# Performance work log

Hardware: AMD Instinct MI355X
Metric: run time of the kernel (lower is better)

## Reference

```python
import jax, jax.numpy as jnp
import numpy as np

B, T, C = 2, 2048, 2048
H, D = 16, 128  # num_heads, head_dim


def setup_inputs() -> dict:
    key = jax.random.key(0)
    ks = jax.random.split(key, 5)
    x = jax.random.normal(ks[0], (B, T, C), dtype=jnp.float32)
    # causal mask: mask==0 positions are filled with -inf
    mask = jnp.tril(jnp.ones((T, T), dtype=jnp.int32))[None, None, :, :]
    wq = jax.random.normal(ks[1], (C, C), dtype=jnp.float32) * (C ** -0.5)
    wk = jax.random.normal(ks[2], (C, C), dtype=jnp.float32) * (C ** -0.5)
    wv = jax.random.normal(ks[3], (C, C), dtype=jnp.float32) * (C ** -0.5)
    wo = jax.random.normal(ks[4], (C, C), dtype=jnp.float32) * (C ** -0.5)
    return {"x": x, "mask": mask, "wq": wq, "wk": wk, "wv": wv, "wo": wo}


def reference(x, mask, wq, wk, wv, wo):
    Bx, Tx, Cx = x.shape
    scale = D ** -0.5
    # torch Linear: y = x @ W.T (weights are [out, in])
    q = (x @ wq.T).reshape(Bx, Tx, H, D).transpose(0, 2, 1, 3)  # [B,H,T,D]
    k = (x @ wk.T).reshape(Bx, Tx, H, D).transpose(0, 2, 1, 3)
    v = (x @ wv.T).reshape(Bx, Tx, H, D).transpose(0, 2, 1, 3)
    scores = jnp.einsum("bhqd,bhkd->bhqk", q, k) * scale  # [B,H,T,T]
    scores = jnp.where(mask == 0, -jnp.inf, scores)
    attn = jax.nn.softmax(scores, axis=-1)
    out = jnp.einsum("bhqk,bhkd->bhqd", attn, v)  # [B,H,T,D]
    out = out.transpose(0, 2, 1, 3).reshape(Bx, Tx, Cx)
    return out @ wo.T
```

## Files before the change

kernel.cpp:

```cpp
#include <hip/hip_runtime.h>
#include <hip/hip_bf16.h>


#define BB 2
#define TT 2048
#define CC 2048
#define HH 16
#define DD 128
#define MM (BB*TT)
#define NQT (TT/64)
#define GNT (CC/64)

typedef __bf16 bf16x8 __attribute__((ext_vector_type(8)));
typedef __bf16 bf16x4 __attribute__((ext_vector_type(4)));
typedef float  f32x4  __attribute__((ext_vector_type(4)));

#define MFMA16(a, b, c) __builtin_amdgcn_mfma_f32_16x16x32_bf16((a), (b), (c), 0, 0, 0)

__device__ __forceinline__ void g2lds16(const void* g, void* l) {
    __builtin_amdgcn_global_load_lds(
        (const __attribute__((address_space(1))) void*)g,
        (__attribute__((address_space(3))) void*)l,
        16, 0, 0);
}

__global__ __launch_bounds__(256) void cvt_all(
    const float* __restrict__ x,  const float* __restrict__ wq,
    const float* __restrict__ wk, const float* __restrict__ wv,
    const float* __restrict__ wo, __bf16* __restrict__ out_base)
{
    const int idx = blockIdx.x * 256 + threadIdx.x;
    const float* in; int off;
    if (idx < (1 << 21)) { in = x; off = idx; }
    else {
        const int r = idx - (1 << 21);
        const int k = r >> 20;
        in  = (k == 0) ? wq : (k == 1) ? wk : (k == 2) ? wv : wo;
        off = r & ((1 << 20) - 1);
    }
    const float4 v = ((const float4*)in)[off];
    bf16x4 o;
    o.x = (__bf16)v.x; o.y = (__bf16)v.y;
    o.z = (__bf16)v.z; o.w = (__bf16)v.w;
    ((bf16x4*)out_base)[idx] = o;
}

template<int MODE>
__global__ __launch_bounds__(512, 2) void gemm_bt(
    const __bf16* __restrict__ A, const __bf16* __restrict__ Wt,
    void* __restrict__ out)
{
    __shared__ __align__(16) __bf16 As[3][256*64];
    __shared__ __align__(16) __bf16 Bs[3][2][128*32];

    const int tid = threadIdx.x;
    const int w   = tid >> 6, lane = tid & 63;
    const int wm  = w >> 1,  wn  = w & 1;
    const int lo  = lane & 15, hi = lane >> 4;
    const int xr  = (lo & 7) << 4;
    const int xb2 = ((lo >> 1) & 3) << 4;

    const int bid   = blockIdx.y * gridDim.x + blockIdx.x;
    const int xcd   = bid & 7, loc = bid >> 3;
    const int n0    = (2*xcd + (loc & 1)) * 128;
    const int m0    = (loc >> 1) * 256;

    const int ar   = tid >> 3, as_ = tid & 7;
    const int acol = ((as_ ^ (ar & 7)) << 3);
    const int br   = tid >> 2, bs_ = tid & 3;
    const int bcol = ((bs_ ^ ((br >> 1) & 3)) << 3);

    auto stageA3a = [&](int buf, int kt) {
        #pragma unroll
        for (int j = 0; j < 3; ++j)
            g2lds16(A + (size_t)(m0 + j*64 + ar)*CC + kt*64 + acol,
                    (char*)&As[buf][0] + j*8192 + w*1024);
    };
    auto stageA3b = [&](int buf, int kt) {
        g2lds16(A + (size_t)(m0 + 3*64 + ar)*CC + kt*64 + acol,
                (char*)&As[buf][0] + 3*8192 + w*1024);
        #pragma unroll
        for (int kh = 0; kh < 2; ++kh)
            g2lds16(Wt + (size_t)(n0 + br)*CC + kt*64 + kh*32 + bcol,
                    (char*)&Bs[buf][kh][0] + w*1024);
    };
    auto rdA = [&](bf16x8* af, int buf, int ks) {
        const char* base = (const char*)&As[buf][0];
        #pragma unroll
        for (int mf = 0; mf < 4; ++mf) {
            const int r = wm*64 + mf*16 + lo;
            af[mf] = *(const bf16x8*)(base + r*128 + ((ks*64 + hi*16) ^ xr));
        }
    };
    auto rdB = [&](bf16x8* bv, int buf, int ks) {
        const char* base = (const char*)&Bs[buf][ks][0];
        #pragma unroll
        for (int nf = 0; nf < 4; ++nf) {
            const int n = wn*64 + nf*16 + lo;
            bv[nf] = *(const bf16x8*)(base + n*64 + ((hi*16) ^ xb2));
        }
    };

    f32x4 acc[4][4] = {};

    stageA3a(0, 0); stageA3b(0, 0);
    stageA3a(1, 1); stageA3b(1, 1);
    asm volatile("s_waitcnt vmcnt(6)" ::: "memory");
    __builtin_amdgcn_s_barrier();

    int rb = 0;
    #pragma unroll 1
    for (int t = 0; t < GNT - 2; ++t) {
        const int sb = (rb == 0) ? 2 : rb - 1;
        {
            bf16x8 af[4], bv[4];
            rdA(af, rb, 0); rdB(bv, rb, 0);
            stageA3a(sb, t + 2);
            __builtin_amdgcn_s_setprio(1);
            #pragma unroll
            for (int mf = 0; mf < 4; ++mf)
                #pragma unroll
                for (int nf = 0; nf < 4; ++nf)
                    acc[mf][nf] = MFMA16(af[mf], bv[nf], acc[mf][nf]);
            __builtin_amdgcn_s_setprio(0);
        }
        {
            bf16x8 af[4], bv[4];
            rdA(af, rb, 1); rdB(bv, rb, 1);
            stageA3b(sb, t + 2);
            __builtin_amdgcn_s_setprio(1);
            #pragma unroll
            for (int mf = 0; mf < 4; ++mf)
                #pragma unroll
                for (int nf = 0; nf < 4; ++nf)
                    acc[mf][nf] = MFMA16(af[mf], bv[nf], acc[mf][nf]);
            __builtin_amdgcn_s_setprio(0);
            asm volatile("s_waitcnt vmcnt(6)" ::: "memory");
            __builtin_amdgcn_s_barrier();
        }
        rb = (rb == 2) ? 0 : rb + 1;
    }
    {
        bf16x8 af[4], bv[4];
        rdA(af, rb, 0); rdB(bv, rb, 0);
        #pragma unroll
        for (int mf = 0; mf < 4; ++mf)
            #pragma unroll
            for (int nf = 0; nf < 4; ++nf)
                acc[mf][nf] = MFMA16(af[mf], bv[nf], acc[mf][nf]);
        rdA(af, rb, 1); rdB(bv, rb, 1);
        #pragma unroll
        for (int mf = 0; mf < 4; ++mf)
            #pragma unroll
            for (int nf = 0; nf < 4; ++nf)
                acc[mf][nf] = MFMA16(af[mf], bv[nf], acc[mf][nf]);
        asm volatile("s_waitcnt vmcnt(0)" ::: "memory");
        __builtin_amdgcn_s_barrier();
        rb = (rb == 2) ? 0 : rb + 1;
    }
    {
        bf16x8 af[4], bv[4];
        rdA(af, rb, 0); rdB(bv, rb, 0);
        #pragma unroll
        for (int mf = 0; mf < 4; ++mf)
            #pragma unroll
            for (int nf = 0; nf < 4; ++nf)
                acc[mf][nf] = MFMA16(af[mf], bv[nf], acc[mf][nf]);
        rdA(af, rb, 1); rdB(bv, rb, 1);
        #pragma unroll
        for (int mf = 0; mf < 4; ++mf)
            #pragma unroll
            for (int nf = 0; nf < 4; ++nf)
                acc[mf][nf] = MFMA16(af[mf], bv[nf], acc[mf][nf]);
    }

    #pragma unroll
    for (int mf = 0; mf < 4; ++mf) {
        #pragma unroll
        for (int nf = 0; nf < 4; ++nf) {
            #pragma unroll
            for (int r = 0; r < 4; ++r) {
                const int row = m0 + wm*64 + mf*16 + hi*4 + r;
                const int col = n0 + wn*64 + nf*16 + lo;
                const float v = acc[mf][nf][r];
                if (MODE == 0) {
                    const int b = row >> 11, t = row & (TT-1);
                    const int h = col >> 7,  d = col & (DD-1);
                    ((__bf16*)out)[(size_t)((b*HH + h)*TT + t)*DD + d] = (__bf16)v;
                } else if (MODE == 1) {
                    const int b = row >> 11, t = row & (TT-1);
                    const int h = col >> 7,  d = col & (DD-1);
                    ((__bf16*)out)[(size_t)((b*HH + h)*DD + d)*TT + t] = (__bf16)v;
                } else {
                    ((float*)out)[(size_t)row*CC + col] = v;
                }
            }
        }
    }
}

__global__ __launch_bounds__(256, 2) void attn_fwd(
    const __bf16* __restrict__ Q, const __bf16* __restrict__ K,
    const __bf16* __restrict__ Vt, __bf16* __restrict__ O)
{
    __shared__ __align__(16) __bf16 Ks[2][64*128];
    __shared__ __align__(16) __bf16 Vs[2][128*64];
    __shared__ __align__(16) __bf16 Ps[4][16*64];

    const int lid   = blockIdx.y * gridDim.x + blockIdx.x;
    const int bh    = lid & 31;
    const int pairx = lid >> 5;
    const int tid = threadIdx.x;
    const int w   = tid >> 6, lane = tid & 63;
    const int lo  = lane & 15, hi = lane >> 4;
    const int xr  = (lo & 7) << 4;

    const int krow_l  = lane >> 4;
    const int kcol_sw = ((lane & 15) << 4);
    const int vrow_l  = lane >> 3;
    const int vcol_sw = (((lane & 7) ^ (lane >> 3)) << 3);

    const size_t kbase = (size_t)bh * TT * DD;
    const size_t vbase = (size_t)bh * DD * TT;
    const int b = bh >> 4, h = bh & 15;
    const float SC = 0.12754613142f;

    bf16x8 vones;
    #pragma unroll
    for (int i = 0; i < 8; ++i) vones[i] = (__bf16)1.0f;

    auto stage = [&](int buf, int kv0) {
        #pragma unroll
        for (int i = 0; i < 4; ++i) {
            const int c = 4*w + i;
            {
                const int row = 4*c + krow_l;
                const int sw  = (kcol_sw ^ ((row & 7) << 4)) >> 1;
                g2lds16(K + kbase + (size_t)(kv0 + row)*DD + sw,
                        &Ks[buf][0] + c*512);
            }
            {
                const int row = 8*c + vrow_l;
                g2lds16(Vt + vbase + (size_t)row*TT + kv0 + vcol_sw,
                        &Vs[buf][0] + c*512);
            }
        }
    };

    #pragma unroll 1
    for (int half = 0; half < 2; ++half) {
        const int qt = half ? pairx : (NQT - 1 - pairx);
        const int q0 = qt * 64;

        const __bf16* Qbase = Q + (kbase + (size_t)(q0 + w*16 + lo) * DD);
        bf16x8 qf[4];
        #pragma unroll
        for (int kc = 0; kc < 4; ++kc)
            qf[kc] = *(const bf16x8*)(Qbase + kc*32 + hi*8);

        float mrow[4];
        #pragma unroll
        for (int r = 0; r < 4; ++r) mrow[r] = -1e30f;
        f32x4 oacc[8] = {};
        f32x4 sacc = {};

        const int qg_base = q0 + w*16 + hi*4;
        const int ntiles  = qt + 1;

        stage(0, 0);
        __syncthreads();
        int cur = 0;

        for (int t = 0; t < ntiles; ++t) {
            const int kv0 = t*64;
            if (t + 1 < ntiles) stage(cur ^ 1, (t+1)*64);

            const char* Kb = (const char*)&Ks[cur][0];
            const char* Vb = (const char*)&Vs[cur][0];

            f32x4 s[4];
            __builtin_amdgcn_s_setprio(1);
            #pragma unroll
            for (int st = 0; st < 4; ++st) {
                f32x4 a = {};
                #pragma unroll
                for (int kc = 0; kc < 4; ++kc) {
                    const bf16x8 kf = *(const bf16x8*)(
                        Kb + (st*16 + lo)*256 + ((kc*64 + hi*16) ^ xr));
                    a = MFMA16(qf[kc], kf, a);
                }
                s[st] = a;
            }
            __builtin_amdgcn_s_setprio(0);

            float pmax[4];
            const bool diag = (t == ntiles - 1);
            #pragma unroll
            for (int r = 0; r < 4; ++r) {
                const int qg = qg_base + r;
                float mx = -1e30f;
                #pragma unroll
                for (int st = 0; st < 4; ++st) {
                    float v = s[st][r] * SC;
                    if (diag) {
                        const int kvg = kv0 + st*16 + lo;
                        v = (kvg > qg) ? -1e30f : v;
                    }
                    s[st][r] = v;
                    mx = fmaxf(mx, v);
                }
                #pragma unroll
                for (int msk = 1; msk < 16; msk <<= 1)
                    mx = fmaxf(mx, __shfl_xor(mx, msk, 64));
                pmax[r] = mx;
            }

            bool need = false;
            #pragma unroll
            for (int r = 0; r < 4; ++r)
                need = need || (pmax[r] > mrow[r] + 11.5f);
            if (__any(need)) {
                float rsc[4];
                #pragma unroll
                for (int r = 0; r < 4; ++r) {
                    const float mnew = fmaxf(mrow[r], pmax[r]);
                    rsc[r]  = __builtin_amdgcn_exp2f(mrow[r] - mnew);
                    mrow[r] = mnew;
                    sacc[r] *= rsc[r];
                }
                #pragma unroll
                for (int dc = 0; dc < 8; ++dc)
                    #pragma unroll
                    for (int r = 0; r < 4; ++r)
                        oacc[dc][r] *= rsc[r];
            }

            #pragma unroll
            for (int r = 0; r < 4; ++r)
                #pragma unroll
                for (int st = 0; st < 4; ++st)
                    s[st][r] = __builtin_amdgcn_exp2f(s[st][r] - mrow[r]);

            char* Pw = (char*)&Ps[w][0];
            #pragma unroll
            for (int st = 0; st < 4; ++st)
                #pragma unroll
                for (int r = 0; r < 4; ++r) {
                    const int row = hi*4 + r;
                    *(__bf16*)(Pw + row*128 + (((st*16 + lo)*2) ^ ((row & 7) << 4)))
                        = (__bf16)s[st][r];
                }

            __builtin_amdgcn_s_setprio(1);
            #pragma unroll
            for (int kc2 = 0; kc2 < 2; ++kc2) {
                const bf16x8 pf = *(const bf16x8*)(
                    Pw + lo*128 + ((kc2*64 + hi*16) ^ xr));
                #pragma unroll
                for (int dc = 0; dc < 8; ++dc) {
                    const bf16x8 vf = *(const bf16x8*)(
                        Vb + (dc*16 + lo)*128 + ((kc2*64 + hi*16) ^ xr));
                    oacc[dc] = MFMA16(pf, vf, oacc[dc]);
                }
                sacc = MFMA16(pf, vones, sacc);
            }
            __builtin_amdgcn_s_setprio(0);

            __syncthreads();
            cur ^= 1;
        }

        #pragma unroll
        for (int r = 0; r < 4; ++r) {
            const float inv = 1.f / sacc[r];
            const int qg = qg_base + r;
            #pragma unroll
            for (int dc = 0; dc < 8; ++dc) {
                const int d = dc*16 + lo;
                O[(size_t)(b*TT + qg)*CC + h*DD + d] = (__bf16)(oacc[dc][r] * inv);
            }
        }
    }
}

extern "C" void kernel_launch(void* const* d_in, const int* in_sizes, int n_in,
                              void* d_out, int out_size, void* d_ws, size_t ws_size,
                              hipStream_t stream) {
    const float* x  = (const float*)d_in[0];
    const float* wq = (const float*)d_in[2];
    const float* wk = (const float*)d_in[3];
    const float* wv = (const float*)d_in[4];
    const float* wo = (const float*)d_in[5];

    char* p = (char*)d_ws;
    __bf16* xb  = (__bf16*)p; p += (size_t)MM*CC*2;
    __bf16* wqb = (__bf16*)p; p += (size_t)CC*CC*2;
    __bf16* wkb = (__bf16*)p; p += (size_t)CC*CC*2;
    __bf16* wvb = (__bf16*)p; p += (size_t)CC*CC*2;
    __bf16* wob = (__bf16*)p; p += (size_t)CC*CC*2;
    __bf16* Qb  = (__bf16*)p; p += (size_t)MM*CC*2;
    __bf16* Kb  = (__bf16*)p; p += (size_t)MM*CC*2;
    __bf16* Vtb = (__bf16*)p; p += (size_t)MM*CC*2;
    __bf16* AOb = xb;

    cvt_all<<<24576, 256, 0, stream>>>(x, wq, wk, wv, wo, xb);

    const dim3 gg(CC/128, MM/256);
    gemm_bt<0><<<gg, 512, 0, stream>>>(xb, wqb, Qb);
    gemm_bt<0><<<gg, 512, 0, stream>>>(xb, wkb, Kb);
    gemm_bt<1><<<gg, 512, 0, stream>>>(xb, wvb, Vtb);

    attn_fwd<<<dim3(NQT/2, BB*HH), 256, 0, stream>>>(Qb, Kb, Vtb, AOb);

    gemm_bt<2><<<gg, 512, 0, stream>>>(AOb, wob, (void*)d_out);
}
```

Measured before the change: 234.8 us.

## Fuse Q and K projections into one 256x256-tile GEMM kernel

Adds a gemm_qk kernel that computes the Q and K projections in one launch over a concatenated weight matrix (wq and wk are contiguous in the workspace) with 256x256 tiles and double-buffered LDS. The epilogue routes each column segment to the Q or K buffer, relying on Qb and Kb being adjacent. This saves a launch and rereads of x, and the larger tile raises arithmetic intensity. In exchange it uses more accumulator registers per thread, which may hurt occupancy. The remaining GEMM launches keep the same grid, now written as a literal.

After: 222.2 us. 1.06x faster.

```diff
diff --git a/kernel.cpp b/kernel.cpp
--- a/kernel.cpp
+++ b/kernel.cpp
@@ -45,6 +45,121 @@
     ((bf16x4*)out_base)[idx] = o;
 }
 
+__global__ __launch_bounds__(512, 2) void gemm_qk(
+    const __bf16* __restrict__ A, const __bf16* __restrict__ Wt,
+    __bf16* __restrict__ out)
+{
+    __shared__ __align__(16) __bf16 As[2][256*64];
+    __shared__ __align__(16) __bf16 Bs[2][2][256*32];
+
+    const int tid = threadIdx.x;
+    const int w   = tid >> 6, lane = tid & 63;
+    const int wm  = w >> 2,  wn  = w & 3;
+    const int lo  = lane & 15, hi = lane >> 4;
+    const int xr  = (lo & 7) << 4;
+    const int xb2 = ((lo >> 1) & 3) << 4;
+
+    const int bid = blockIdx.y * gridDim.x + blockIdx.x;
+    const int xcd = bid & 7, loc = bid >> 3;
+    const int n0  = (2*xcd + (loc & 1)) * 256;
+    const int m0  = (loc >> 1) * 256;
+
+    const int ar   = tid >> 3, as_ = tid & 7;
+    const int acol = ((as_ ^ (ar & 7)) << 3);
+    const int brr  = tid >> 2, bs_ = tid & 3;
+    const int bcol = ((bs_ ^ ((brr >> 1) & 3)) << 3);
+
+    auto stageA = [&](int buf, int kt) {
+        #pragma unroll
+        for (int j = 0; j < 4; ++j)
+            g2lds16(A + (size_t)(m0 + j*64 + ar)*CC + kt*64 + acol,
+                    (char*)&As[buf][0] + j*8192 + w*1024);
+    };
+    auto stageB = [&](int buf, int kt) {
+        #pragma unroll
+        for (int ks = 0; ks < 2; ++ks)
+            #pragma unroll
+            for (int jb = 0; jb < 2; ++jb)
+                g2lds16(Wt + (size_t)(n0 + jb*128 + brr)*CC + kt*64 + ks*32 + bcol,
+                        (char*)&Bs[buf][ks][0] + jb*8192 + w*1024);
+    };
+    auto rdA = [&](bf16x8* af, int buf, int ks) {
+        const char* base = (const char*)&As[buf][0];
+        #pragma unroll
+        for (int mf = 0; mf < 8; ++mf) {
+            const int r = wm*128 + mf*16 + lo;
+            af[mf] = *(const bf16x8*)(base + r*128 + ((ks*64 + hi*16) ^ xr));
+        }
+    };
+    auto rdB = [&](bf16x8* bv, int buf, int ks) {
+        const char* base = (const char*)&Bs[buf][ks][0];
+        #pragma unroll
+        for (int nf = 0; nf < 4; ++nf) {
+            const int n = wn*64 + nf*16 + lo;
+            bv[nf] = *(const bf16x8*)(base + n*64 + ((hi*16) ^ xb2));
+        }
+    };
+
+    f32x4 acc[8][4] = {};
+
+    stageA(0, 0); stageB(0, 0);
+    asm volatile("s_waitcnt vmcnt(0)" ::: "memory");
+    __builtin_amdgcn_s_barrier();
+
+    int buf = 0;
+    #pragma unroll 1
+    for (int t = 0; t < GNT; ++t) {
+        const bool hn = (t + 1 < GNT);
+        {
+            bf16x8 af[8], bv[4];
+            rdA(af, buf, 0); rdB(bv, buf, 0);
+            if (hn) stageA(buf ^ 1, t + 1);
+            __builtin_amdgcn_s_setprio(1);
+            #pragma unroll
+            for (int mf = 0; mf < 8; ++mf)
+                #pragma unroll
+                for (int nf = 0; nf < 4; ++nf)
+                    acc[mf][nf] = MFMA16(af[mf], bv[nf], acc[mf][nf]);
+            __builtin_amdgcn_s_setprio(0);
+        }
+        {
+            bf16x8 af[8], bv[4];
+            rdA(af, buf, 1); rdB(bv, buf, 1);
+            if (hn) stageB(buf ^ 1, t + 1);
+            __builtin_amdgcn_s_setprio(1);
+            #pragma unroll
+            for (int mf = 0; mf < 8; ++mf)
+                #pragma unroll
+                for (int nf = 0; nf < 4; ++nf)
+                    acc[mf][nf] = MFMA16(af[mf], bv[nf], acc[mf][nf]);
+            __builtin_amdgcn_s_setprio(0);
+            if (hn) {
+                asm volatile("s_waitcnt vmcnt(0)" ::: "memory");
+                __builtin_amdgcn_s_barrier();
+            }
+        }
+        buf ^= 1;
+    }
+
+    #pragma unroll
+    for (int mf = 0; mf < 8; ++mf) {
+        #pragma unroll
+        for (int nf = 0; nf < 4; ++nf) {
+            #pragma unroll
+            for (int r = 0; r < 4; ++r) {
+                const int row = m0 + wm*128 + mf*16 + hi*4 + r;
+                const int col = n0 + wn*64 + nf*16 + lo;
+                const int seg = col >> 11;
+                const int c2  = col & (CC-1);
+                const int b = row >> 11, t_ = row & (TT-1);
+                const int h = c2 >> 7,  d  = c2 & (DD-1);
+                __bf16* dst = out + (size_t)seg * MM * CC;
+                dst[(size_t)((b*HH + h)*TT + t_)*DD + d] = (__bf16)acc[mf][nf][r];
+            }
+        }
+    }
+}
+
 template<int MODE>
 __global__ __launch_bounds__(512, 2) void gemm_bt(
     const __bf16* __restrict__ A, const __bf16* __restrict__ Wt,
@@ -183,11 +298,7 @@
                 const int row = m0 + wm*64 + mf*16 + hi*4 + r;
                 const int col = n0 + wn*64 + nf*16 + lo;
                 const float v = acc[mf][nf][r];
-                if (MODE == 0) {
-                    const int b = row >> 11, t = row & (TT-1);
-                    const int h = col >> 7,  d = col & (DD-1);
-                    ((__bf16*)out)[(size_t)((b*HH + h)*TT + t)*DD + d] = (__bf16)v;
-                } else if (MODE == 1) {
+                if (MODE == 1) {
                     const int b = row >> 11, t = row & (TT-1);
                     const int h = col >> 7,  d = col & (DD-1);
                     ((__bf16*)out)[(size_t)((b*HH + h)*DD + d)*TT + t] = (__bf16)v;
@@ -402,15 +513,14 @@
     __bf16* Kb  = (__bf16*)p; p += (size_t)MM*CC*2;
     __bf16* Vtb = (__bf16*)p; p += (size_t)MM*CC*2;
     __bf16* AOb = xb;
+    (void)wkb;
 
     cvt_all<<<24576, 256, 0, stream>>>(x, wq, wk, wv, wo, xb);
 
-    const dim3 gg(CC/128, MM/256);
-    gemm_bt<0><<<gg, 512, 0, stream>>>(xb, wqb, Qb);
-    gemm_bt<0><<<gg, 512, 0, stream>>>(xb, wkb, Kb);
-    gemm_bt<1><<<gg, 512, 0, stream>>>(xb, wvb, Vtb);
+    gemm_qk<<<dim3(16, 16), 512, 0, stream>>>(xb, wqb, Qb);
+    gemm_bt<1><<<dim3(16, 16), 512, 0, stream>>>(xb, wvb, Vtb);
 
     attn_fwd<<<dim3(NQT/2, BB*HH), 256, 0, stream>>>(Qb, Kb, Vtb, AOb);
 
-    gemm_bt<2><<<gg, 512, 0, stream>>>(AOb, wob, (void*)d_out);
+    gemm_bt<2><<<dim3(16, 16), 512, 0, stream>>>(AOb, wob, (void*)d_out);
 }
```
